# Performance work log

Measured on AMD Instinct MI355X. Metric: run time of the kernel, lower is better.

## Reference

```python
import jax, jax.numpy as jnp
import numpy as np

N = 50000        # nodes
E = 250000       # edges (first N are self-loops -> every node has in-degree >= 1)
H = 12           # num_heads
D = 64           # per-head dim (in_dim == out_dim == 64)
NEG_SLOPE = 0.2  # LeakyReLU alpha


def setup_inputs() -> dict:
    key = jax.random.key(0)
    k1, k2, k3, k4, k5, k6, k7 = jax.random.split(key, 7)
    h = jax.random.normal(k1, (N, H * D), dtype=jnp.float32)
    # self-loops + random in-neighbors so segment softmax is well defined for all dst
    src = jnp.concatenate([jnp.arange(N, dtype=jnp.int32),
                           jax.random.randint(k2, (E - N,), 0, N, dtype=jnp.int32)])
    dst = jnp.concatenate([jnp.arange(N, dtype=jnp.int32),
                           jax.random.randint(k3, (E - N,), 0, N, dtype=jnp.int32)])
    xav = 1.414 / np.sqrt(D)  # ~ xavier_normal gain=1.414
    W_fc = jax.random.normal(k4, (D, D), dtype=jnp.float32) * xav
    attn_l = jax.random.normal(k5, (H, D), dtype=jnp.float32) * 0.15
    attn_r = jax.random.normal(k6, (H, D), dtype=jnp.float32) * 0.15
    W_res = jax.random.normal(k7, (D, D), dtype=jnp.float32) * xav
    return {"h": h, "W_fc": W_fc, "attn_l": attn_l, "attn_r": attn_r,
            "W_res": W_res, "src": src, "dst": dst}


def reference(h, W_fc, attn_l, attn_r, W_res, src, dst):
    n = h.shape[0]
    hh = h.reshape(n, H, D)                              # [N,H,D]
    # fc is Linear(D, D, bias=False) shared across heads: y = x @ W^T
    ft = jnp.einsum('nhd,ed->nhe', hh, W_fc)             # [N,H,D]
    a1 = jnp.einsum('nhd,hd->nh', ft, attn_l)            # [N,H]
    a2 = jnp.einsum('nhd,hd->nh', ft, attn_r)            # [N,H]
    # edge_attention: leaky_relu(src.a1 + dst.a2)
    e = jax.nn.leaky_relu(a1[src] + a2[dst], negative_slope=NEG_SLOPE)  # [E,H]
    # segment softmax over incoming edges per destination node (stable)
    m = jax.ops.segment_max(e, dst, num_segments=n)       # [N,H]
    ee = jnp.exp(e - m[dst])                              # [E,H]
    denom = jax.ops.segment_sum(ee, dst, num_segments=n)  # [N,H]
    alpha = ee / denom[dst]                               # [E,H]
    # message: alpha * src ft, scatter-sum into dst
    agg = jax.ops.segment_sum(alpha[:, :, None] * ft[src], dst, num_segments=n)  # [N,H,D]
    # residual: res_fc(h) per head, then ReLU(flatten)
    res = jnp.einsum('nhd,ed->nhe', hh, W_res)            # [N,H,D]
    return jax.nn.relu((res + agg).reshape(n, H * D))     # [N,768]
```

## Files before the change

### kernel.cpp

```cpp
#include <hip/hip_runtime.h>
#include <hip/hip_bf16.h>

#define N_NODES 50000
#define N_EDGES 250000
#define NHEAD   12
#define NH      (N_NODES * NHEAD)
#define ROW_TILES (NH / 16)

typedef __bf16 bf16_t;
typedef __bf16 bf16x8 __attribute__((ext_vector_type(8)));
typedef __bf16 bf16x4 __attribute__((ext_vector_type(4)));
typedef float  f32x4  __attribute__((ext_vector_type(4)));

__device__ __forceinline__ bf16x8 cvt8(f32x4 a, f32x4 b) {
    bf16x8 r;
    r[0] = (bf16_t)a[0]; r[1] = (bf16_t)a[1]; r[2] = (bf16_t)a[2]; r[3] = (bf16_t)a[3];
    r[4] = (bf16_t)b[0]; r[5] = (bf16_t)b[1]; r[6] = (bf16_t)b[2]; r[7] = (bf16_t)b[3];
    return r;
}

__global__ __launch_bounds__(256) void k_deg_prep(
    const int* __restrict__ dst, int* __restrict__ deg,
    const float* __restrict__ wfc, const float* __restrict__ wres,
    const float* __restrict__ attl, const float* __restrict__ attr,
    bf16_t* __restrict__ wfb, bf16_t* __restrict__ wrb,
    bf16_t* __restrict__ ulb, bf16_t* __restrict__ urb)
{
    int b = blockIdx.x;
    if (b < 245) {
        int i4 = b * 256 + threadIdx.x;
        if (i4 < N_EDGES / 4) {
            int4 q = reinterpret_cast<const int4*>(dst)[i4];
            atomicAdd(&deg[q.x], 1);
            atomicAdd(&deg[q.y], 1);
            atomicAdd(&deg[q.z], 1);
            atomicAdd(&deg[q.w], 1);
        }
    } else if (b < 261) {
        int t = (b - 245) * 256 + threadIdx.x;
        wfb[t] = (bf16_t)wfc[t];
        wrb[t] = (bf16_t)wres[t];
    } else if (b < 265) {
        int u = (b - 261) * 256 + threadIdx.x;
        int hh = u >> 6, d = u & 63;
        float s = 0.f;
        if (hh < NHEAD) {
#pragma unroll 8
            for (int e = 0; e < 64; ++e) s += attl[hh * 64 + e] * wfc[e * 64 + d];
        }
        ulb[u] = (bf16_t)s;
    } else {
        int u = (b - 265) * 256 + threadIdx.x;
        int hh = u >> 6, d = u & 63;
        float s = 0.f;
        if (hh < NHEAD) {
#pragma unroll 8
            for (int e = 0; e < 64; ++e) s += attr[hh * 64 + e] * wfc[e * 64 + d];
        }
        urb[u] = (bf16_t)s;
    }
}

__global__ __launch_bounds__(1024) void k_scan(const int* __restrict__ deg,
                                               int* __restrict__ rowptr,
                                               int* __restrict__ cursor) {
    __shared__ int s[1024];
    const int CH = 52;
    int t = threadIdx.x;
    int base = t * CH;
    int loc[CH];
    if (base + CH <= N_NODES) {
        const int4* p = reinterpret_cast<const int4*>(deg + base);
#pragma unroll
        for (int i = 0; i < CH / 4; ++i) {
            int4 q = p[i];
            loc[4 * i + 0] = q.x; loc[4 * i + 1] = q.y;
            loc[4 * i + 2] = q.z; loc[4 * i + 3] = q.w;
        }
    } else {
#pragma unroll
        for (int i = 0; i < CH; ++i) {
            int idx = base + i;
            loc[i] = (idx < N_NODES) ? deg[idx] : 0;
        }
    }
    int sum = 0;
#pragma unroll
    for (int i = 0; i < CH; ++i) sum += loc[i];
    s[t] = sum;
    __syncthreads();
    for (int off = 1; off < 1024; off <<= 1) {
        int v = (t >= off) ? s[t - off] : 0;
        __syncthreads();
        s[t] += v;
        __syncthreads();
    }
    int run = s[t] - sum;
#pragma unroll
    for (int i = 0; i < CH; ++i) {
        int idx = base + i;
        if (idx < N_NODES) {
            rowptr[idx] = run;
            cursor[idx] = run;
            run += loc[i];
        }
    }
    if (t == 1023) rowptr[N_NODES] = s[1023];
}

__global__ __launch_bounds__(256) void k_fill_gemm(
    const int* __restrict__ src, const int* __restrict__ dst,
    int* __restrict__ cursor, int* __restrict__ csr_src,
    const float* __restrict__ h,
    const bf16_t* __restrict__ wfb,
    const bf16_t* __restrict__ wrb,
    const bf16_t* __restrict__ ulb,
    const bf16_t* __restrict__ urb,
    bf16_t* __restrict__ ft,
    bf16_t* __restrict__ resb,
    float* __restrict__ al,
    float* __restrict__ ar)
{
    __shared__ bf16_t sb[4][2][16 * 72];
    if (blockIdx.x < 977) {
        int i = blockIdx.x * 256 + threadIdx.x;
        if (i < N_EDGES) {
            int d = dst[i];
            int pos = atomicAdd(&cursor[d], 1);
            csr_src[pos] = src[i];
        }
        return;
    }
    int bid  = blockIdx.x - 977;
    int wv   = threadIdx.x >> 6;
    int lane = threadIdx.x & 63;
    int lr = lane & 15, lg = lane >> 4;
    int l8 = lane & 7,  lrow = lane >> 3;
    bf16_t* fs = &sb[wv][0][0];
    bf16_t* rs = &sb[wv][1][0];

    const f32x4*  hv  = reinterpret_cast<const f32x4*>(h);
    const bf16x8* wf  = reinterpret_cast<const bf16x8*>(wfb);
    const bf16x8* wr  = reinterpret_cast<const bf16x8*>(wrb);
    const bf16x8* ulv = reinterpret_cast<const bf16x8*>(ulb);
    const bf16x8* urv = reinterpret_cast<const bf16x8*>(urb);
    bf16x8 ul0 = ulv[lr * 8 + lg], ul1 = ulv[lr * 8 + 4 + lg];
    bf16x8 ur0 = urv[lr * 8 + lg], ur1 = urv[lr * 8 + 4 + lg];

    const int nw = 1875 * 4;
    int tile = bid * 4 + wv;

    f32x4 c0, c1, c2, c3;
    if (tile < ROW_TILES) {
        int ab = (tile * 16 + lr) * 16 + lg * 2;
        c0 = hv[ab];     c1 = hv[ab + 1];
        c2 = hv[ab + 8]; c3 = hv[ab + 9];
    }
    while (tile < ROW_TILES) {
        int nxt = tile + nw;
        f32x4 n0, n1, n2, n3;
        if (nxt < ROW_TILES) {
            int ab = (nxt * 16 + lr) * 16 + lg * 2;
            n0 = hv[ab];     n1 = hv[ab + 1];
            n2 = hv[ab + 8]; n3 = hv[ab + 9];
        }
        bf16x8 a0 = cvt8(c0, c1), a1 = cvt8(c2, c3);
        int r0 = tile << 4;
        int r  = r0 + lr;
        int hh = r % NHEAD;

        f32x4 dl = {0.f, 0.f, 0.f, 0.f}, dr = {0.f, 0.f, 0.f, 0.f};
        dl = __builtin_amdgcn_mfma_f32_16x16x32_bf16(ul0, a0, dl, 0, 0, 0);
        dl = __builtin_amdgcn_mfma_f32_16x16x32_bf16(ul1, a1, dl, 0, 0, 0);
        dr = __builtin_amdgcn_mfma_f32_16x16x32_bf16(ur0, a0, dr, 0, 0, 0);
        dr = __builtin_amdgcn_mfma_f32_16x16x32_bf16(ur1, a1, dr, 0, 0, 0);
        if (lg == (hh >> 2)) {
#pragma unroll
            for (int j = 0; j < 4; ++j)
                if ((hh & 3) == j) { al[r] = dl[j]; ar[r] = dr[j]; }
        }

#pragma unroll
        for (int nt = 0; nt < 4; ++nt) {
            int brow = (nt * 16 + lr) * 8;
            f32x4 z = {0.f, 0.f, 0.f, 0.f};
            z = __builtin_amdgcn_mfma_f32_16x16x32_bf16(wf[brow + lg],     a0, z, 0, 0, 0);
            z = __builtin_amdgcn_mfma_f32_16x16x32_bf16(wf[brow + 4 + lg], a1, z, 0, 0, 0);
            f32x4 y = {0.f, 0.f, 0.f, 0.f};
            y = __builtin_amdgcn_mfma_f32_16x16x32_bf16(wr[brow + lg],     a0, y, 0, 0, 0);
            y = __builtin_amdgcn_mfma_f32_16x16x32_bf16(wr[brow + 4 + lg], a1, y, 0, 0, 0);
            bf16x4 pf, pe;
#pragma unroll
            for (int j = 0; j < 4; ++j) { pf[j] = (bf16_t)z[j]; pe[j] = (bf16_t)y[j]; }
            *reinterpret_cast<bf16x4*>(fs + lr * 72 + nt * 16 + lg * 4) = pf;
            *reinterpret_cast<bf16x4*>(rs + lr * 72 + nt * 16 + lg * 4) = pe;
        }

#pragma unroll
        for (int k = 0; k < 2; ++k) {
            int row = lrow + k * 8;
            bf16x8 vf = *reinterpret_cast<const bf16x8*>(fs + row * 72 + l8 * 8);
            bf16x8 vr = *reinterpret_cast<const bf16x8*>(rs + row * 72 + l8 * 8);
            *reinterpret_cast<bf16x8*>(ft   + (r0 + row) * 64 + l8 * 8) = vf;
            *reinterpret_cast<bf16x8*>(resb + (r0 + row) * 64 + l8 * 8) = vr;
        }

        c0 = n0; c1 = n1; c2 = n2; c3 = n3;
        tile = nxt;
    }
}

#define DB 4
__global__ __launch_bounds__(256) void k_agg(
    const int* __restrict__ rowptr, const int* __restrict__ csr_src,
    const float* __restrict__ al, const float* __restrict__ ar,
    const bf16_t* __restrict__ ft, const bf16_t* __restrict__ resb,
    float* __restrict__ out)
{
    int d0 = (blockIdx.x * 256 + threadIdx.x) >> 6;
    d0 = __builtin_amdgcn_readfirstlane(d0);
    if (d0 >= N_NODES) return;
    int l  = threadIdx.x & 63;
    int hA = l >> 3;
    int hB = 8 + (l >> 4);
    int u_l = l / 12;
    int h_l = l - u_l * 12;
    int beg = rowptr[d0], end = rowptr[d0 + 1];
    float arW = 0.f;
    if (l < 48) arW = ar[d0 * NHEAD + h_l];

    float accA[8] = {0,0,0,0,0,0,0,0};
    float accB[4] = {0,0,0,0};
    float denA = 0.f, denB = 0.f;

    for (int j0 = beg; j0 < end; j0 += DB) {
        int idx[DB];
#pragma unroll
        for (int u = 0; u < DB; ++u) {
            int j = j0 + u;
            idx[u] = csr_src[(j < end) ? j : beg];
        }
        float wv = 0.f;
        {
            int e = idx[0];
            e = (u_l == 1) ? idx[1] : e;
            e = (u_l == 2) ? idx[2] : e;
            e = (u_l == 3) ? idx[3] : e;
            if (l < 48) {
                float x = al[e * NHEAD + h_l] + arW;
                x = (x > 0.f) ? x : 0.2f * x;
                wv = ((j0 + u_l) < end) ? __expf(x) : 0.f;
            }
        }
        float wA[DB], wB[DB];
#pragma unroll
        for (int u = 0; u < DB; ++u) {
            wA[u] = __shfl(wv, u * 12 + hA, 64);
            wB[u] = __shfl(wv, u * 12 + hB, 64);
        }
        bf16x8 vA[DB]; bf16x4 vB[DB];
#pragma unroll
        for (int u = 0; u < DB; ++u) {
            const bf16_t* row = ft + idx[u] * 768;
            vA[u] = *reinterpret_cast<const bf16x8*>(row + 8 * l);
            vB[u] = *reinterpret_cast<const bf16x4*>(row + 512 + 4 * l);
        }
#pragma unroll
        for (int u = 0; u < DB; ++u) {
            denA += wA[u]; denB += wB[u];
#pragma unroll
            for (int k = 0; k < 8; ++k) accA[k] += wA[u] * (float)vA[u][k];
#pragma unroll
            for (int k = 0; k < 4; ++k) accB[k] += wB[u] * (float)vB[u][k];
        }
    }

    const bf16_t* rrow = resb + d0 * 768;
    bf16x8 rA = *reinterpret_cast<const bf16x8*>(rrow + 8 * l);
    bf16x4 rB = *reinterpret_cast<const bf16x4*>(rrow + 512 + 4 * l);
    float* orow = out + d0 * 768;
    f32x4 o0, o1, o2;
    float ia = 1.f / denA, ib = 1.f / denB;
#pragma unroll
    for (int k = 0; k < 4; ++k) {
        float x = (float)rA[k] + accA[k] * ia;         o0[k] = x > 0.f ? x : 0.f;
        float y = (float)rA[k + 4] + accA[k + 4] * ia; o1[k] = y > 0.f ? y : 0.f;
        float z = (float)rB[k] + accB[k] * ib;         o2[k] = z > 0.f ? z : 0.f;
    }
    __builtin_nontemporal_store(o0, reinterpret_cast<f32x4*>(orow + 8 * l));
    __builtin_nontemporal_store(o1, reinterpret_cast<f32x4*>(orow + 8 * l + 4));
    __builtin_nontemporal_store(o2, reinterpret_cast<f32x4*>(orow + 512 + 4 * l));
}

extern "C" void kernel_launch(void* const* d_in, const int* in_sizes, int n_in,
                              void* d_out, int out_size, void* d_ws, size_t ws_size,
                              hipStream_t stream) {
    const float* h    = (const float*)d_in[0];
    const float* wfc  = (const float*)d_in[1];
    const float* attl = (const float*)d_in[2];
    const float* attr = (const float*)d_in[3];
    const float* wres = (const float*)d_in[4];
    const int*   src  = (const int*)d_in[5];
    const int*   dst  = (const int*)d_in[6];
    float* out = (float*)d_out;

    char* ws = (char*)d_ws;
    bf16_t* ft     = (bf16_t*)(ws + 0);
    bf16_t* resb   = (bf16_t*)(ws + 76800000);
    float*  al     = (float*)(ws + 153600000);
    float*  ar     = (float*)(ws + 156000000);
    int*    deg    = (int*)(ws + 158400000);
    int*    rowptr = (int*)(ws + 158600448);
    int*    cursor = (int*)(ws + 158800896);
    int*    csrsrc = (int*)(ws + 159001344);
    bf16_t* wfb    = (bf16_t*)(ws + 160001344);
    bf16_t* wrb    = (bf16_t*)(ws + 160009536);
    bf16_t* ulb    = (bf16_t*)(ws + 160017728);
    bf16_t* urb    = (bf16_t*)(ws + 160019776);

    (void)hipMemsetAsync(deg, 0, N_NODES * sizeof(int), stream);
    k_deg_prep<<<269, 256, 0, stream>>>(dst, deg, wfc, wres, attl, attr, wfb, wrb, ulb, urb);
    k_scan<<<1, 1024, 0, stream>>>(deg, rowptr, cursor);
    k_fill_gemm<<<977 + 1875, 256, 0, stream>>>(src, dst, cursor, csrsrc,
                                                h, wfb, wrb, ulb, urb, ft, resb, al, ar);
    k_agg<<<(N_NODES + 3) / 4, 256, 0, stream>>>(rowptr, csrsrc, al, ar, ft, resb, out);
}
```

Measured before the change: 238.0 us.

## Drop rowptr via post-fill cursor, reorder blocks, nontemporal loads, deeper agg batch

```diff
diff --git a/kernel.cpp b/kernel.cpp
--- a/kernel.cpp
+++ b/kernel.cpp
@@ -62,7 +62,6 @@
 }
 
 __global__ __launch_bounds__(1024) void k_scan(const int* __restrict__ deg,
-                                               int* __restrict__ rowptr,
                                                int* __restrict__ cursor) {
     __shared__ int s[1024];
     const int CH = 52;
@@ -100,12 +99,10 @@
     for (int i = 0; i < CH; ++i) {
         int idx = base + i;
         if (idx < N_NODES) {
-            rowptr[idx] = run;
             cursor[idx] = run;
             run += loc[i];
         }
     }
-    if (t == 1023) rowptr[N_NODES] = s[1023];
 }
 
 __global__ __launch_bounds__(256) void k_fill_gemm(
@@ -122,8 +119,8 @@
     float* __restrict__ ar)
 {
     __shared__ bf16_t sb[4][2][16 * 72];
-    if (blockIdx.x < 977) {
-        int i = blockIdx.x * 256 + threadIdx.x;
+    if (blockIdx.x >= 1875) {
+        int i = (blockIdx.x - 1875) * 256 + threadIdx.x;
         if (i < N_EDGES) {
             int d = dst[i];
             int pos = atomicAdd(&cursor[d], 1);
@@ -131,7 +128,7 @@
         }
         return;
     }
-    int bid  = blockIdx.x - 977;
+    int bid  = blockIdx.x;
     int wv   = threadIdx.x >> 6;
     int lane = threadIdx.x & 63;
     int lr = lane & 15, lg = lane >> 4;
@@ -153,16 +150,20 @@
     f32x4 c0, c1, c2, c3;
     if (tile < ROW_TILES) {
         int ab = (tile * 16 + lr) * 16 + lg * 2;
-        c0 = hv[ab];     c1 = hv[ab + 1];
-        c2 = hv[ab + 8]; c3 = hv[ab + 9];
+        c0 = __builtin_nontemporal_load(hv + ab);
+        c1 = __builtin_nontemporal_load(hv + ab + 1);
+        c2 = __builtin_nontemporal_load(hv + ab + 8);
+        c3 = __builtin_nontemporal_load(hv + ab + 9);
     }
     while (tile < ROW_TILES) {
         int nxt = tile + nw;
         f32x4 n0, n1, n2, n3;
         if (nxt < ROW_TILES) {
             int ab = (nxt * 16 + lr) * 16 + lg * 2;
-            n0 = hv[ab];     n1 = hv[ab + 1];
-            n2 = hv[ab + 8]; n3 = hv[ab + 9];
+            n0 = __builtin_nontemporal_load(hv + ab);
+            n1 = __builtin_nontemporal_load(hv + ab + 1);
+            n2 = __builtin_nontemporal_load(hv + ab + 8);
+            n3 = __builtin_nontemporal_load(hv + ab + 9);
         }
         bf16x8 a0 = cvt8(c0, c1), a1 = cvt8(c2, c3);
         int r0 = tile << 4;
@@ -210,9 +211,9 @@
     }
 }
 
-#define DB 4
+#define DB 8
 __global__ __launch_bounds__(256) void k_agg(
-    const int* __restrict__ rowptr, const int* __restrict__ csr_src,
+    const int* __restrict__ cur, const int* __restrict__ csr_src,
     const float* __restrict__ al, const float* __restrict__ ar,
     const bf16_t* __restrict__ ft, const bf16_t* __restrict__ resb,
     float* __restrict__ out)
@@ -225,7 +226,8 @@
     int hB = 8 + (l >> 4);
     int u_l = l / 12;
     int h_l = l - u_l * 12;
-    int beg = rowptr[d0], end = rowptr[d0 + 1];
+    int beg = d0 ? cur[d0 - 1] : 0;
+    int end = cur[d0];
     float arW = 0.f;
     if (l < 48) arW = ar[d0 * NHEAD + h_l];
 
@@ -240,23 +242,28 @@
             int j = j0 + u;
             idx[u] = csr_src[(j < end) ? j : beg];
         }
-        float wv = 0.f;
+        float wv0 = 0.f, wv1 = 0.f;
         {
-            int e = idx[0];
-            e = (u_l == 1) ? idx[1] : e;
-            e = (u_l == 2) ? idx[2] : e;
-            e = (u_l == 3) ? idx[3] : e;
+            int e0 = idx[0], e1 = idx[4];
+            e0 = (u_l == 1) ? idx[1] : e0;  e1 = (u_l == 1) ? idx[5] : e1;
+            e0 = (u_l == 2) ? idx[2] : e0;  e1 = (u_l == 2) ? idx[6] : e1;
+            e0 = (u_l == 3) ? idx[3] : e0;  e1 = (u_l == 3) ? idx[7] : e1;
             if (l < 48) {
-                float x = al[e * NHEAD + h_l] + arW;
-                x = (x > 0.f) ? x : 0.2f * x;
-                wv = ((j0 + u_l) < end) ? __expf(x) : 0.f;
+                float x0 = al[e0 * NHEAD + h_l] + arW;
+                float x1 = al[e1 * NHEAD + h_l] + arW;
+                x0 = (x0 > 0.f) ? x0 : 0.2f * x0;
+                x1 = (x1 > 0.f) ? x1 : 0.2f * x1;
+                wv0 = ((j0 + u_l)     < end) ? __expf(x0) : 0.f;
+                wv1 = ((j0 + 4 + u_l) < end) ? __expf(x1) : 0.f;
             }
         }
         float wA[DB], wB[DB];
 #pragma unroll
-        for (int u = 0; u < DB; ++u) {
-            wA[u] = __shfl(wv, u * 12 + hA, 64);
-            wB[u] = __shfl(wv, u * 12 + hB, 64);
+        for (int u = 0; u < 4; ++u) {
+            wA[u]     = __shfl(wv0, u * 12 + hA, 64);
+            wB[u]     = __shfl(wv0, u * 12 + hB, 64);
+            wA[u + 4] = __shfl(wv1, u * 12 + hA, 64);
+            wB[u + 4] = __shfl(wv1, u * 12 + hB, 64);
         }
         bf16x8 vA[DB]; bf16x4 vB[DB];
 #pragma unroll
@@ -276,8 +283,8 @@
     }
 
     const bf16_t* rrow = resb + d0 * 768;
-    bf16x8 rA = *reinterpret_cast<const bf16x8*>(rrow + 8 * l);
-    bf16x4 rB = *reinterpret_cast<const bf16x4*>(rrow + 512 + 4 * l);
+    bf16x8 rA = __builtin_nontemporal_load(reinterpret_cast<const bf16x8*>(rrow + 8 * l));
+    bf16x4 rB = __builtin_nontemporal_load(reinterpret_cast<const bf16x4*>(rrow + 512 + 4 * l));
     float* orow = out + d0 * 768;
     f32x4 o0, o1, o2;
     float ia = 1.f / denA, ib = 1.f / denB;
@@ -310,7 +317,6 @@
     float*  al     = (float*)(ws + 153600000);
     float*  ar     = (float*)(ws + 156000000);
     int*    deg    = (int*)(ws + 158400000);
-    int*    rowptr = (int*)(ws + 158600448);
     int*    cursor = (int*)(ws + 158800896);
     int*    csrsrc = (int*)(ws + 159001344);
     bf16_t* wfb    = (bf16_t*)(ws + 160001344);
@@ -320,8 +326,8 @@
 
     (void)hipMemsetAsync(deg, 0, N_NODES * sizeof(int), stream);
     k_deg_prep<<<269, 256, 0, stream>>>(dst, deg, wfc, wres, attl, attr, wfb, wrb, ulb, urb);
-    k_scan<<<1, 1024, 0, stream>>>(deg, rowptr, cursor);
-    k_fill_gemm<<<977 + 1875, 256, 0, stream>>>(src, dst, cursor, csrsrc,
+    k_scan<<<1, 1024, 0, stream>>>(deg, cursor);
+    k_fill_gemm<<<1875 + 977, 256, 0, stream>>>(src, dst, cursor, csrsrc,
                                                 h, wfb, wrb, ulb, urb, ft, resb, al, ar);
-    k_agg<<<(N_NODES + 3) / 4, 256, 0, stream>>>(rowptr, csrsrc, al, ar, ft, resb, out);
-}
+    k_agg<<<(N_NODES + 3) / 4, 256, 0, stream>>>(cursor, csrsrc, al, ar, ft, resb, out);
+}
```

Result: faster. 209.6 us, median of 2 (-11.9%).
